# Optimization experiments

Hardware: AMD Instinct MI355X
Metric: run time of the kernel (lower is better)

The kernel has to match this reference:

```python
import math
import jax, jax.numpy as jnp
import numpy as np

jax.config.update("jax_enable_x64", True)  # torch hash math is int64

L = 16
F = 2
T = 524288
PRIMES = (1, 2654435761, 805459861)
N_MIN = 16
N_MAX = 2048
_b = math.exp((math.log(N_MAX) - math.log(N_MIN)) / (L - 1))
RESOLUTIONS = [math.floor(N_MIN * _b ** i) for i in range(L)]
# corner index bits: bit2 -> x offset, bit1 -> y, bit0 -> z (matches torch buffer)
OFFSETS = jnp.array([[0, 0, 0], [0, 0, 1], [0, 1, 0], [0, 1, 1],
                     [1, 0, 0], [1, 0, 1], [1, 1, 0], [1, 1, 1]], dtype=jnp.int64)


def setup_inputs() -> dict:
    key = jax.random.key(0)
    k1, k2 = jax.random.split(key)
    x = jax.random.uniform(k1, (2097152, 3), dtype=jnp.float32)  # coords in [0,1)
    embeddings = jax.random.uniform(k2, (L, T, F), minval=-1e-4, maxval=1e-4,
                                    dtype=jnp.float32)
    return {"x": x, "embeddings": embeddings}


def _encode(x, embeddings):
    feats = []
    for i, res in enumerate(RESOLUTIONS):
        xs = x * res                               # [N,3]
        xf = xs.astype(jnp.int64)                  # trunc == floor for nonneg
        w = xs - xf.astype(x.dtype)                # [N,3] trilinear weights
        fx, fy, fz = w[:, 0:1], w[:, 1:2], w[:, 2:3]  # [N,1] each
        c = xf[:, None, :] + OFFSETS[None, :, :]   # [N,8,3]
        h = ((c[..., 0] * PRIMES[0])
             ^ (c[..., 1] * PRIMES[1])
             ^ (c[..., 2] * PRIMES[2])) % T        # [N,8]
        corners = embeddings[i][h]                 # [N,8,F] gather
        c00 = corners[:, 0] * (1 - fx) + corners[:, 4] * fx
        c01 = corners[:, 1] * (1 - fx) + corners[:, 5] * fx
        c10 = corners[:, 2] * (1 - fx) + corners[:, 6] * fx
        c11 = corners[:, 3] * (1 - fx) + corners[:, 7] * fx
        c0 = c00 * (1 - fy) + c10 * fy
        c1 = c01 * (1 - fy) + c11 * fy
        feats.append(c0 * (1 - fz) + c1 * fz)      # [N,F]
    return jnp.concatenate(feats, axis=-1)         # [N, L*F]


def reference(x, embeddings):
    return _encode(x, embeddings)
```

## Files before the change

kernel.cpp:

```cpp
#include <hip/hip_runtime.h>
#include <cmath>

#define L_LEVELS 16
#define T_SIZE 524288u
#define T_MASK (T_SIZE - 1u)
#define P1 2654435761u
#define P2 805459861u

#define NBB   5
#define NB1   (1 << NBB)
#define NBINS (1 << (3 * NBB))

struct ResArr { int r[L_LEVELS]; };
typedef float f32x4 __attribute__((ext_vector_type(4)));

__device__ __forceinline__ float2 encode_point(
    float px, float py, float pz, float rf,
    const float2* __restrict__ E, const float4* __restrict__ E4)
{
    const float sx = px * rf, sy = py * rf, sz = pz * rf;
    const int ix = (int)sx, iy = (int)sy, iz = (int)sz;
    const float fx = sx - (float)ix;
    const float fy = sy - (float)iy;
    const float fz = sz - (float)iz;

    const unsigned hx0 = (unsigned)ix,      hx1 = hx0 + 1u;
    const unsigned hy0 = (unsigned)iy * P1, hy1 = hy0 + P1;
    const unsigned hz0 = (unsigned)iz * P2, hz1 = hz0 + P2;
    const unsigned diffx = hx0 ^ hx1;

    const unsigned h0 = (hx0 ^ hy0 ^ hz0) & T_MASK;
    const unsigned h1 = (hx0 ^ hy0 ^ hz1) & T_MASK;
    const unsigned h2 = (hx0 ^ hy1 ^ hz0) & T_MASK;
    const unsigned h3 = (hx0 ^ hy1 ^ hz1) & T_MASK;

    float2 c0v, c1v, c2v, c3v, c4v, c5v, c6v, c7v;

    if (diffx == 1u) {
        const float4 v0 = E4[h0 >> 1];
        const float4 v1 = E4[h1 >> 1];
        const float4 v2 = E4[h2 >> 1];
        const float4 v3 = E4[h3 >> 1];
        const bool o0 = (h0 & 1u), o1 = (h1 & 1u), o2 = (h2 & 1u), o3 = (h3 & 1u);
        c0v = o0 ? make_float2(v0.z, v0.w) : make_float2(v0.x, v0.y);
        c1v = o1 ? make_float2(v1.z, v1.w) : make_float2(v1.x, v1.y);
        c2v = o2 ? make_float2(v2.z, v2.w) : make_float2(v2.x, v2.y);
        c3v = o3 ? make_float2(v3.z, v3.w) : make_float2(v3.x, v3.y);
        c4v = o0 ? make_float2(v0.x, v0.y) : make_float2(v0.z, v0.w);
        c5v = o1 ? make_float2(v1.x, v1.y) : make_float2(v1.z, v1.w);
        c6v = o2 ? make_float2(v2.x, v2.y) : make_float2(v2.z, v2.w);
        c7v = o3 ? make_float2(v3.x, v3.y) : make_float2(v3.z, v3.w);
    } else {
        c0v = E[h0];
        c1v = E[h1];
        c2v = E[h2];
        c3v = E[h3];
        c4v = E[h0 ^ diffx];
        c5v = E[h1 ^ diffx];
        c6v = E[h2 ^ diffx];
        c7v = E[h3 ^ diffx];
    }

    const float gx = 1.0f - fx, gy = 1.0f - fy, gz = 1.0f - fz;
    const float c00x = c0v.x * gx + c4v.x * fx;
    const float c00y = c0v.y * gx + c4v.y * fx;
    const float c01x = c1v.x * gx + c5v.x * fx;
    const float c01y = c1v.y * gx + c5v.y * fx;
    const float c10x = c2v.x * gx + c6v.x * fx;
    const float c10y = c2v.y * gx + c6v.y * fx;
    const float c11x = c3v.x * gx + c7v.x * fx;
    const float c11y = c3v.y * gx + c7v.y * fx;

    const float a0x = c00x * gy + c10x * fy;
    const float a0y = c00y * gy + c10y * fy;
    const float a1x = c01x * gy + c11x * fy;
    const float a1y = c01y * gy + c11y * fy;

    return make_float2(a0x * gz + a1x * fz, a0y * gz + a1y * fz);
}

__device__ __forceinline__ unsigned bin_key(float px, float py, float pz)
{
    int bx = (int)(px * (float)NB1); bx = bx > NB1 - 1 ? NB1 - 1 : bx;
    int by = (int)(py * (float)NB1); by = by > NB1 - 1 ? NB1 - 1 : by;
    int bz = (int)(pz * (float)NB1); bz = bz > NB1 - 1 ? NB1 - 1 : bz;
    return (((unsigned)bz << NBB | (unsigned)by) << NBB) | (unsigned)bx;
}

__global__ __launch_bounds__(256) void hist_kernel(
    const float* __restrict__ x, unsigned* __restrict__ hist, int npts)
{
    int i = blockIdx.x * 256 + threadIdx.x;
    const int stride = gridDim.x * 256;
    for (; i < npts; i += stride) {
        const size_t b = (size_t)i * 3;
        atomicAdd(&hist[bin_key(x[b], x[b + 1], x[b + 2])], 1u);
    }
}

__global__ __launch_bounds__(1024) void scan_kernel(unsigned* __restrict__ hist)
{
    __shared__ unsigned wsum[16];
    const int t = threadIdx.x;
    const int CH = NBINS / 1024;
    unsigned v[NBINS / 1024];
    unsigned s = 0;
    #pragma unroll
    for (int j = 0; j < CH; ++j) { v[j] = hist[t * CH + j]; s += v[j]; }

    unsigned inc = s;
    #pragma unroll
    for (int d = 1; d < 64; d <<= 1) {
        const unsigned n = __shfl_up(inc, d, 64);
        if ((t & 63) >= d) inc += n;
    }
    const int wave = t >> 6;
    if ((t & 63) == 63) wsum[wave] = inc;
    __syncthreads();
    if (wave == 0) {
        const unsigned w = (t < 16) ? wsum[t] : 0u;
        unsigned winc = w;
        #pragma unroll
        for (int d = 1; d < 16; d <<= 1) {
            const unsigned n = __shfl_up(winc, d, 64);
            if (t >= d) winc += n;
        }
        if (t < 16) wsum[t] = winc - w;
    }
    __syncthreads();

    unsigned run = wsum[wave] + (inc - s);
    #pragma unroll
    for (int j = 0; j < CH; ++j) { const unsigned tmp = v[j]; hist[t * CH + j] = run; run += tmp; }
}

__global__ __launch_bounds__(256) void scatter_kernel(
    const float* __restrict__ x, unsigned* __restrict__ cursor,
    float4* __restrict__ xs4, int npts)
{
    __shared__ float xsh[768];
    const int tid = threadIdx.x, pbase = blockIdx.x * 256;
    if (pbase + 256 <= npts) {
        if (tid < 192)
            ((float4*)xsh)[tid] = ((const float4*)(x + (size_t)pbase * 3))[tid];
    } else {
        const int nfl = npts * 3 - pbase * 3;
        for (int i = tid; i < nfl; i += 256) xsh[i] = x[(size_t)pbase * 3 + i];
    }
    __syncthreads();
    const int p = pbase + tid;
    if (p >= npts) return;
    const float px = xsh[tid * 3], py = xsh[tid * 3 + 1], pz = xsh[tid * 3 + 2];
    const unsigned dest = atomicAdd(&cursor[bin_key(px, py, pz)], 1u);
    xs4[dest] = make_float4(px, py, pz, __uint_as_float((unsigned)p));
}

__global__ __launch_bounds__(256) void enc_level_sorted(
    const float4* __restrict__ xs4,
    const float* __restrict__ emb,
    float2* __restrict__ ws,
    ResArr res, int npts)
{
    const int level = blockIdx.y;
    const int p = blockIdx.x * 256 + threadIdx.x;
    if (p >= npts) return;
    const float4 q = xs4[p];
    const float rf = (float)res.r[level];
    const float2* __restrict__ E  = (const float2*)emb + (size_t)level * T_SIZE;
    const float4* __restrict__ E4 = (const float4*)E;
    const float2 r = encode_point(q.x, q.y, q.z, rf, E, E4);
    union { float2 f2; double d; } u; u.f2 = r;
    __builtin_nontemporal_store(u.d, (double*)&ws[(size_t)level * npts + p]);
}

__global__ __launch_bounds__(256) void transpose_unperm_kernel(
    const float2* __restrict__ ws, const float4* __restrict__ xs4,
    float4* __restrict__ out4, int npts)
{
    __shared__ float2 tile[256 * 17];
    __shared__ unsigned pidx[256];
    const int t = threadIdx.x, pbase = blockIdx.x * 256;
    const double* __restrict__ wsd = (const double*)ws;

    if (pbase + 256 <= npts) {
        #pragma unroll
        for (int l = 0; l < L_LEVELS; ++l) {
            const double tmp =
                __builtin_nontemporal_load(&wsd[(size_t)l * npts + pbase + t]);
            *(double*)&tile[t * 17 + l] = tmp;
        }
        pidx[t] = __float_as_uint(((const float*)xs4)[4 * (size_t)(pbase + t) + 3]);
        __syncthreads();

        #pragma unroll
        for (int pass = 0; pass < 8; ++pass) {
            const int r = pass * 32 + (t >> 3);
            const int q = t & 7;
            const size_t prow = (size_t)pidx[r];
            const float2 a = tile[r * 17 + 2 * q];
            const float2 b = tile[r * 17 + 2 * q + 1];
            f32x4 v; v.x = a.x; v.y = a.y; v.z = b.x; v.w = b.y;
            __builtin_nontemporal_store(v, (f32x4*)&out4[prow * 8 + q]);
        }
    } else {
        const int p = pbase + t;
        if (p < npts) {
            #pragma unroll
            for (int l = 0; l < L_LEVELS; ++l)
                tile[t * 17 + l] = ws[(size_t)l * npts + p];
            pidx[t] = __float_as_uint(((const float*)xs4)[4 * (size_t)p + 3]);
        }
        __syncthreads();
        if (p < npts) {
            const size_t prow = (size_t)pidx[t];
            for (int k = 0; k < 8; ++k) {
                const float2 a = tile[t * 17 + 2 * k];
                const float2 b = tile[t * 17 + 2 * k + 1];
                out4[prow * 8 + k] = make_float4(a.x, a.y, b.x, b.y);
            }
        }
    }
}

__global__ __launch_bounds__(256) void enc_level_kernel(
    const float* __restrict__ x,
    const float* __restrict__ emb,
    float2* __restrict__ ws,
    ResArr res, int npts)
{
    __shared__ float xsh[768];
    const int tid   = threadIdx.x;
    const int level = blockIdx.y;
    const int pbase = blockIdx.x * 256;

    if (pbase + 256 <= npts) {
        if (tid < 192)
            ((float4*)xsh)[tid] = ((const float4*)(x + (size_t)pbase * 3))[tid];
    } else {
        const int nfl = npts * 3 - pbase * 3;
        for (int i = tid; i < nfl; i += 256) xsh[i] = x[(size_t)pbase * 3 + i];
    }
    __syncthreads();

    const int p = pbase + tid;
    if (p >= npts) return;

    const float rf = (float)res.r[level];
    const float2* __restrict__ E  = (const float2*)emb + (size_t)level * T_SIZE;
    const float4* __restrict__ E4 = (const float4*)E;

    const float2 r = encode_point(xsh[tid * 3 + 0], xsh[tid * 3 + 1],
                                  xsh[tid * 3 + 2], rf, E, E4);
    ws[(size_t)level * npts + p] = r;
}

__global__ __launch_bounds__(256) void transpose_tile_kernel(
    const float2* __restrict__ ws, float4* __restrict__ out4, int npts)
{
    __shared__ float2 tile[256 * 17];
    const int t     = threadIdx.x;
    const int pbase = blockIdx.x * 256;

    if (pbase + 256 <= npts) {
        #pragma unroll
        for (int l = 0; l < L_LEVELS; ++l)
            tile[t * 17 + l] = ws[(size_t)l * npts + pbase + t];
        __syncthreads();
        #pragma unroll
        for (int i = 0; i < 8; ++i) {
            const int jl = i * 256 + t;
            const int pl = jl >> 3;
            const int k  = jl & 7;
            const float2 a = tile[pl * 17 + 2 * k];
            const float2 b = tile[pl * 17 + 2 * k + 1];
            out4[(size_t)pbase * 8 + jl] = make_float4(a.x, a.y, b.x, b.y);
        }
    } else {
        const int p = pbase + t;
        if (p < npts) {
            #pragma unroll
            for (int l = 0; l < L_LEVELS; ++l)
                tile[t * 17 + l] = ws[(size_t)l * npts + p];
        }
        __syncthreads();
        const int npts_loc = npts - pbase;
        for (int i = 0; i < 8; ++i) {
            const int jl = i * 256 + t;
            const int pl = jl >> 3;
            const int k  = jl & 7;
            if (pl < npts_loc) {
                const float2 a = tile[pl * 17 + 2 * k];
                const float2 b = tile[pl * 17 + 2 * k + 1];
                out4[(size_t)pbase * 8 + jl] = make_float4(a.x, a.y, b.x, b.y);
            }
        }
    }
}

__global__ __launch_bounds__(256) void hash_enc_fallback(
    const float* __restrict__ x,
    const float* __restrict__ emb,
    float* __restrict__ out,
    ResArr res, int npts)
{
    __shared__ float xsh[48];
    const int tid = threadIdx.x;
    const int blockPointBase = blockIdx.x * 16;
    if (tid < 48) xsh[tid] = x[(size_t)blockPointBase * 3 + tid];
    __syncthreads();

    const int lp    = tid >> 4;
    const int level = tid & 15;
    const int p     = blockPointBase + lp;
    if (p >= npts) return;

    const float rf = (float)res.r[level];
    const float2* __restrict__ E  = (const float2*)emb + (size_t)level * T_SIZE;
    const float4* __restrict__ E4 = (const float4*)E;

    const float2 r = encode_point(xsh[lp * 3 + 0], xsh[lp * 3 + 1],
                                  xsh[lp * 3 + 2], rf, E, E4);
    ((float2*)out)[(size_t)p * 16 + level] = r;
}

extern "C" void kernel_launch(void* const* d_in, const int* in_sizes, int n_in,
                              void* d_out, int out_size, void* d_ws, size_t ws_size,
                              hipStream_t stream) {
    const float* x   = (const float*)d_in[0];
    const float* emb = (const float*)d_in[1];

    ResArr res;
    const double b = exp((log(2048.0) - log(16.0)) / 15.0);
    for (int i = 0; i < L_LEVELS; ++i)
        res.r[i] = (int)floor(16.0 * pow(b, (double)i));

    const int npts = in_sizes[0] / 3;
    const int pblocks = (npts + 255) / 256;

    const size_t ws2_bytes  = (size_t)npts * L_LEVELS * sizeof(float2);
    const size_t xs4_bytes  = (size_t)npts * sizeof(float4);
    const size_t hist_bytes = (size_t)NBINS * sizeof(unsigned);
    const size_t need_sorted = ws2_bytes + xs4_bytes + hist_bytes;

    if (ws_size >= need_sorted) {
        float2*   ws2  = (float2*)d_ws;
        float4*   xs4  = (float4*)((char*)d_ws + ws2_bytes);
        unsigned* hist = (unsigned*)((char*)d_ws + ws2_bytes + xs4_bytes);

        hipMemsetAsync(hist, 0, hist_bytes, stream);
        hipLaunchKernelGGL(hist_kernel, dim3(2048), dim3(256), 0, stream,
                           x, hist, npts);
        hipLaunchKernelGGL(scan_kernel, dim3(1), dim3(1024), 0, stream, hist);
        hipLaunchKernelGGL(scatter_kernel, dim3(pblocks), dim3(256), 0, stream,
                           x, hist, xs4, npts);
        hipLaunchKernelGGL(enc_level_sorted, dim3(pblocks, L_LEVELS), dim3(256),
                           0, stream, xs4, emb, ws2, res, npts);
        hipLaunchKernelGGL(transpose_unperm_kernel, dim3(pblocks), dim3(256),
                           0, stream, ws2, xs4, (float4*)d_out, npts);
    } else if (ws_size >= ws2_bytes) {
        float2* ws = (float2*)d_ws;
        hipLaunchKernelGGL(enc_level_kernel, dim3(pblocks, L_LEVELS), dim3(256),
                           0, stream, x, emb, ws, res, npts);
        hipLaunchKernelGGL(transpose_tile_kernel, dim3(pblocks), dim3(256),
                           0, stream, ws, (float4*)d_out, npts);
    } else {
        const int blocks = (npts + 15) / 16;
        hipLaunchKernelGGL(hash_enc_fallback, dim3(blocks), dim3(256),
                           0, stream, x, emb, (float*)d_out, res, npts);
    }
}
```

Measured before the change: 1.119 ms.

## Fuse coarse hash-grid levels into the unpermute/transpose kernel

The eight coarsest levels are now encoded directly inside the transpose/unpermute kernel, so their results go straight to shared memory instead of a workspace round trip. Only the eight finer levels still run in the level-parallel sorted kernel and go through global memory. This halves workspace writes and reads and shrinks the workspace. The cost is a heavier serial loop per thread in the transpose kernel, which may expose gather latency and lower occupancy there.

```diff
diff --git a/kernel.cpp b/kernel.cpp
--- a/kernel.cpp
+++ b/kernel.cpp
@@ -2,6 +2,7 @@
 #include <cmath>
 
 #define L_LEVELS 16
+#define LSPLIT   8
 #define T_SIZE 524288u
 #define T_MASK (T_SIZE - 1u)
 #define P1 2654435761u
@@ -161,7 +162,7 @@
     float2* __restrict__ ws,
     ResArr res, int npts)
 {
-    const int level = blockIdx.y;
+    const int level = LSPLIT + blockIdx.y;
     const int p = blockIdx.x * 256 + threadIdx.x;
     if (p >= npts) return;
     const float4 q = xs4[p];
@@ -170,12 +171,14 @@
     const float4* __restrict__ E4 = (const float4*)E;
     const float2 r = encode_point(q.x, q.y, q.z, rf, E, E4);
     union { float2 f2; double d; } u; u.f2 = r;
-    __builtin_nontemporal_store(u.d, (double*)&ws[(size_t)level * npts + p]);
+    __builtin_nontemporal_store(u.d,
+        (double*)&ws[(size_t)(level - LSPLIT) * npts + p]);
 }
 
 __global__ __launch_bounds__(256) void transpose_unperm_kernel(
     const float2* __restrict__ ws, const float4* __restrict__ xs4,
-    float4* __restrict__ out4, int npts)
+    const float* __restrict__ emb,
+    float4* __restrict__ out4, ResArr res, int npts)
 {
     __shared__ float2 tile[256 * 17];
     __shared__ unsigned pidx[256];
@@ -183,32 +186,49 @@
     const double* __restrict__ wsd = (const double*)ws;
 
     if (pbase + 256 <= npts) {
-        #pragma unroll
-        for (int l = 0; l < L_LEVELS; ++l) {
-            const double tmp =
-                __builtin_nontemporal_load(&wsd[(size_t)l * npts + pbase + t]);
+        const float4 q = xs4[pbase + t];
+        pidx[t] = __float_as_uint(q.w);
+
+        #pragma unroll
+        for (int l = LSPLIT; l < L_LEVELS; ++l) {
+            const double tmp = __builtin_nontemporal_load(
+                &wsd[(size_t)(l - LSPLIT) * npts + pbase + t]);
             *(double*)&tile[t * 17 + l] = tmp;
         }
-        pidx[t] = __float_as_uint(((const float*)xs4)[4 * (size_t)(pbase + t) + 3]);
+        #pragma unroll 1
+        for (int l = 0; l < LSPLIT; ++l) {
+            const float rf = (float)res.r[l];
+            const float2* E  = (const float2*)emb + (size_t)l * T_SIZE;
+            const float4* E4 = (const float4*)E;
+            tile[t * 17 + l] = encode_point(q.x, q.y, q.z, rf, E, E4);
+        }
         __syncthreads();
 
         #pragma unroll
         for (int pass = 0; pass < 8; ++pass) {
             const int r = pass * 32 + (t >> 3);
-            const int q = t & 7;
+            const int k = t & 7;
             const size_t prow = (size_t)pidx[r];
-            const float2 a = tile[r * 17 + 2 * q];
-            const float2 b = tile[r * 17 + 2 * q + 1];
+            const float2 a = tile[r * 17 + 2 * k];
+            const float2 b = tile[r * 17 + 2 * k + 1];
             f32x4 v; v.x = a.x; v.y = a.y; v.z = b.x; v.w = b.y;
-            __builtin_nontemporal_store(v, (f32x4*)&out4[prow * 8 + q]);
+            __builtin_nontemporal_store(v, (f32x4*)&out4[prow * 8 + k]);
         }
     } else {
         const int p = pbase + t;
+        float4 q = make_float4(0.f, 0.f, 0.f, 0.f);
         if (p < npts) {
-            #pragma unroll
-            for (int l = 0; l < L_LEVELS; ++l)
-                tile[t * 17 + l] = ws[(size_t)l * npts + p];
-            pidx[t] = __float_as_uint(((const float*)xs4)[4 * (size_t)p + 3]);
+            q = xs4[p];
+            pidx[t] = __float_as_uint(q.w);
+            for (int l = LSPLIT; l < L_LEVELS; ++l)
+                tile[t * 17 + l] = ws[(size_t)(l - LSPLIT) * npts + p];
+            #pragma unroll 1
+            for (int l = 0; l < LSPLIT; ++l) {
+                const float rf = (float)res.r[l];
+                const float2* E  = (const float2*)emb + (size_t)l * T_SIZE;
+                const float4* E4 = (const float4*)E;
+                tile[t * 17 + l] = encode_point(q.x, q.y, q.z, rf, E, E4);
+            }
         }
         __syncthreads();
         if (p < npts) {
@@ -337,10 +357,11 @@
     const int npts = in_sizes[0] / 3;
     const int pblocks = (npts + 255) / 256;
 
-    const size_t ws2_bytes  = (size_t)npts * L_LEVELS * sizeof(float2);
+    const size_t ws2_bytes  = (size_t)npts * (L_LEVELS - LSPLIT) * sizeof(float2);
     const size_t xs4_bytes  = (size_t)npts * sizeof(float4);
     const size_t hist_bytes = (size_t)NBINS * sizeof(unsigned);
     const size_t need_sorted = ws2_bytes + xs4_bytes + hist_bytes;
+    const size_t ws_full    = (size_t)npts * L_LEVELS * sizeof(float2);
 
     if (ws_size >= need_sorted) {
         float2*   ws2  = (float2*)d_ws;
@@ -353,11 +374,12 @@
         hipLaunchKernelGGL(scan_kernel, dim3(1), dim3(1024), 0, stream, hist);
         hipLaunchKernelGGL(scatter_kernel, dim3(pblocks), dim3(256), 0, stream,
                            x, hist, xs4, npts);
-        hipLaunchKernelGGL(enc_level_sorted, dim3(pblocks, L_LEVELS), dim3(256),
+        hipLaunchKernelGGL(enc_level_sorted,
+                           dim3(pblocks, L_LEVELS - LSPLIT), dim3(256),
                            0, stream, xs4, emb, ws2, res, npts);
         hipLaunchKernelGGL(transpose_unperm_kernel, dim3(pblocks), dim3(256),
-                           0, stream, ws2, xs4, (float4*)d_out, npts);
-    } else if (ws_size >= ws2_bytes) {
+                           0, stream, ws2, xs4, emb, (float4*)d_out, res, npts);
+    } else if (ws_size >= ws_full) {
         float2* ws = (float2*)d_ws;
         hipLaunchKernelGGL(enc_level_kernel, dim3(pblocks, L_LEVELS), dim3(256),
                            0, stream, x, emb, ws, res, npts);
```

Measured after the change: 1.051 ms. -6.1%, faster.
